# Performance work log

Measured on AMD Instinct MI355X. Metric: run time of the kernel, lower is better.

## Reference

```python
import jax, jax.numpy as jnp
import numpy as np

N, E, G = 100000, 800000, 1
DV, DE, DU, H = 64, 32, 32, 128

def _w(key, shape):
    return jax.random.normal(key, shape, dtype=jnp.float32) * 0.05

def setup_inputs() -> dict:
    key = jax.random.key(0)
    ks = jax.random.split(key, 16)
    inp = {
        "node_attr": jax.random.normal(ks[0], (N, DV), dtype=jnp.float32),
        "edges": jax.random.randint(ks[1], (2, E), 0, N, dtype=jnp.int64 if jax.config.jax_enable_x64 else jnp.int32),
        "edge_attr": jax.random.normal(ks[2], (E, DE), dtype=jnp.float32),
        "u": jax.random.normal(ks[3], (G, DU), dtype=jnp.float32),
        "node_idx": jnp.zeros((N,), dtype=jnp.int32),
        "edge_idx": jnp.zeros((E,), dtype=jnp.int32),
        # edge MLP: concat(src, dst, edge_attr, u) -> H -> H
        "W1e": _w(ks[4], (2 * DV + DE + DU, H)), "b1e": jnp.zeros((H,), jnp.float32),
        "W2e": _w(ks[5], (H, H)), "b2e": jnp.zeros((H,), jnp.float32),
        # node MLP: concat(node_attr, aggregated_edges, u) -> H -> H
        "W1n": _w(ks[6], (DV + H + DU, H)), "b1n": jnp.zeros((H,), jnp.float32),
        "W2n": _w(ks[7], (H, H)), "b2n": jnp.zeros((H,), jnp.float32),
        # global MLP: concat(node_mean, edge_mean, u) -> H -> H
        "W1g": _w(ks[8], (H + H + DU, H)), "b1g": jnp.zeros((H,), jnp.float32),
        "W2g": _w(ks[9], (H, H)), "b2g": jnp.zeros((H,), jnp.float32),
    }
    return inp

def _mlp(x, W1, b1, W2, b2):
    return jax.nn.relu(x @ W1 + b1) @ W2 + b2

def _seg_mean(x, seg, num):
    s = jax.ops.segment_sum(x, seg, num_segments=num)
    c = jax.ops.segment_sum(jnp.ones((x.shape[0], 1), x.dtype), seg, num_segments=num)
    return s / jnp.maximum(c, 1.0)

def reference(node_attr, edges, edge_attr, u, node_idx, edge_idx,
              W1e, b1e, W2e, b2e, W1n, b1n, W2n, b2n, W1g, b1g, W2g, b2g):
    row, col = edges[0], edges[1]
    # edge model: gather endpoint features, concat with edge/global attrs
    e_in = jnp.concatenate([node_attr[row], node_attr[col], edge_attr, u[edge_idx]], axis=-1)
    e = _mlp(e_in, W1e, b1e, W2e, b2e)                        # [E, H]
    # node model: scatter-add incoming edge messages onto receivers (col)
    agg = jax.ops.segment_sum(e, col, num_segments=node_attr.shape[0])  # [N, H]
    v_in = jnp.concatenate([node_attr, agg, u[node_idx]], axis=-1)
    v = _mlp(v_in, W1n, b1n, W2n, b2n)                        # [N, H]
    # global model: per-graph mean pooling of nodes and edges
    nv = _seg_mean(v, node_idx, u.shape[0])                   # [G, H]
    ne = _seg_mean(e, edge_idx, u.shape[0])                   # [G, H]
    g_in = jnp.concatenate([nv, ne, u], axis=-1)
    g = _mlp(g_in, W1g, b1g, W2g, b2g)                        # [G, H]
    return v, e, g
```

## Files before the change

kernel.cpp:

```cpp
#include <hip/hip_runtime.h>

#define N_NODES 100000
#define N_EDGES 800000
#define DV 64
#define DE 32
#define DU 32
#define H 128

#define ETILE 128
#define NTILES_E (N_EDGES / ETILE)

typedef short bf16x8 __attribute__((ext_vector_type(8)));
typedef unsigned short u16;
typedef u16 u16x8 __attribute__((ext_vector_type(8)));
typedef float f32x4 __attribute__((ext_vector_type(4)));

#define OFF_ESUM 0
#define OFF_VSUM 8192
#define OFF_BIAS 16384
#define OFF_PART 17408
#define OFF_WBUF 19456
#define OFF_DEG  175104
#define OFF_OFFS 575104
#define OFF_BUCK 975104

#define W1ET_OFF 0
#define W2ET_OFF 20480
#define W1NT_OFF 36864
#define W2NT_OFF 61440
#define WBUF_ELEMS 77824

#define NPART 391

__device__ inline u16 f2bf(float x) {
  union { float f; unsigned u; } c; c.f = x;
  unsigned r = c.u + 0x7FFFu + ((c.u >> 16) & 1u);
  return (u16)(r >> 16);
}

__global__ void prep_weights(const float* __restrict__ W1e, const float* __restrict__ W2e,
                             const float* __restrict__ W1n, const float* __restrict__ W2n,
                             u16* __restrict__ wbuf) {
  int i = blockIdx.x * blockDim.x + threadIdx.x;
  if (i < 20480) {
    int j = i / 160, k = i - j * 160;
    wbuf[W1ET_OFF + i] = f2bf(W1e[k * H + j]);
  } else if (i < 36864) {
    int t = i - 20480; int j = t >> 7, k = t & 127;
    wbuf[i] = f2bf(W2e[k * H + j]);
  } else if (i < 61440) {
    int t = i - 36864; int j = t / 192, k = t - j * 192;
    wbuf[i] = f2bf(W1n[k * H + j]);
  } else if (i < WBUF_ELEMS) {
    int t = i - 61440; int j = t >> 7, k = t & 127;
    wbuf[i] = f2bf(W2n[k * H + j]);
  }
}

__global__ void prep_bias(const float* __restrict__ uattr,
                          const float* __restrict__ W1e, const float* __restrict__ b1e,
                          const float* __restrict__ W1n, const float* __restrict__ b1n,
                          float* __restrict__ bias) {
  int t = threadIdx.x;
  float be = b1e[t];
  float bn = b1n[t];
  for (int k = 0; k < DU; ++k) {
    float uk = uattr[k];
    be += uk * W1e[(2 * DV + DE + k) * H + t];
    bn += uk * W1n[(DV + H + k) * H + t];
  }
  bias[t] = be;
  bias[128 + t] = bn;
}

__global__ void degree_kernel(const int* __restrict__ edges, int* __restrict__ deg) {
  int i = blockIdx.x * 256 + threadIdx.x;
  if (i < N_EDGES) atomicAdd(&deg[edges[N_EDGES + i]], 1);
}

__global__ void scan_part(const int* __restrict__ deg, int* __restrict__ part) {
  int i = blockIdx.x * 256 + threadIdx.x;
  int v = (i < N_NODES) ? deg[i] : 0;
#pragma unroll
  for (int m = 1; m < 64; m <<= 1) v += __shfl_xor(v, m);
  __shared__ int s[4];
  if ((threadIdx.x & 63) == 0) s[threadIdx.x >> 6] = v;
  __syncthreads();
  if (threadIdx.x == 0) part[blockIdx.x] = s[0] + s[1] + s[2] + s[3];
}

__global__ void scan_top(int* __restrict__ part) {
  __shared__ int s[512];
  int t = threadIdx.x;
  s[t] = (t < NPART) ? part[t] : 0;
  __syncthreads();
  for (int d = 1; d < 512; d <<= 1) {
    int v = (t >= d) ? s[t - d] : 0;
    __syncthreads();
    s[t] += v;
    __syncthreads();
  }
  if (t < NPART) part[t] = (t == 0) ? 0 : s[t - 1];
}

__global__ void scan_down(const int* __restrict__ part, int* __restrict__ deg_cursor,
                          int* __restrict__ offsets) {
  __shared__ int s[256];
  int b = blockIdx.x, t = threadIdx.x;
  int i = b * 256 + t;
  int v = (i < N_NODES) ? deg_cursor[i] : 0;
  s[t] = v;
  __syncthreads();
  for (int d = 1; d < 256; d <<= 1) {
    int u = (t >= d) ? s[t - d] : 0;
    __syncthreads();
    s[t] += u;
    __syncthreads();
  }
  int excl = s[t] - v + part[b];
  if (i < N_NODES) { offsets[i] = excl; deg_cursor[i] = excl; }
}

__global__ void fill_kernel(const int* __restrict__ edges, int* __restrict__ cursor,
                            int* __restrict__ bucket) {
  int i = blockIdx.x * 256 + threadIdx.x;
  if (i < N_EDGES) {
    int d = edges[N_EDGES + i];
    int pos = atomicAdd(&cursor[d], 1);
    bucket[pos] = i;
  }
}

__global__ __launch_bounds__(512, 2) void edge_kernel(
    const float* __restrict__ node_attr, const int* __restrict__ edges,
    const float* __restrict__ edge_attr,
    const u16* __restrict__ wbuf, const float* __restrict__ bias_f,
    const float* __restrict__ b2,
    float* __restrict__ e_out, float* __restrict__ esum_p)
{
  __shared__ __align__(16) char smem[75776];
  u16 (*X)[164]    = (u16(*)[164])smem;
  u16 (*Hs)[132]   = (u16(*)[132])(smem + 41984);
  float (*OT)[132] = (float(*)[132])smem;
  __shared__ int sSrc[128], sDst[128];

  const int tid = threadIdx.x;
  const int wave = tid >> 6, lane = tid & 63;
  const int l15 = lane & 15, lg = lane >> 4;
  const int wc = (wave & 3) * 32;
  const int rh = (wave >> 2) * 64;
  const long e0 = (long)blockIdx.x * ETILE;

  if (tid < 128)       sSrc[tid]       = edges[e0 + tid];
  else if (tid < 256)  sDst[tid - 128] = edges[(long)N_EDGES + e0 + (tid - 128)];

  bf16x8 w1[5][2];
  {
    const u16* w1t = wbuf + W1ET_OFF;
#pragma unroll
    for (int cf = 0; cf < 2; ++cf) {
      const u16* p1 = w1t + (wc + cf * 16 + l15) * 160 + lg * 8;
#pragma unroll
      for (int ks = 0; ks < 5; ++ks) w1[ks][cf] = *(const bf16x8*)(p1 + ks * 32);
    }
  }
  float bias1[2] = { bias_f[wc + l15], bias_f[wc + 16 + l15] };

  __syncthreads();

  {
    float4 g0[5], g1[5];
    int r_[5], c_[5];
#pragma unroll
    for (int it = 0; it < 5; ++it) {
      int ch = tid + it * 512;
      int r = ch / 20, gseg = ch - r * 20;
      int col = gseg * 8;
      r_[it] = r; c_[it] = col;
      const float* src;
      if (col < 64)        src = node_attr + (long)sSrc[r] * DV + col;
      else if (col < 128)  src = node_attr + (long)sDst[r] * DV + (col - 64);
      else                 src = edge_attr + (e0 + r) * DE + (col - 128);
      g0[it] = *(const float4*)src;
      g1[it] = *(const float4*)(src + 4);
    }
#pragma unroll
    for (int it = 0; it < 5; ++it) {
      u16x8 p;
      p[0] = f2bf(g0[it].x); p[1] = f2bf(g0[it].y); p[2] = f2bf(g0[it].z); p[3] = f2bf(g0[it].w);
      p[4] = f2bf(g1[it].x); p[5] = f2bf(g1[it].y); p[6] = f2bf(g1[it].z); p[7] = f2bf(g1[it].w);
      *(u16x8*)&X[r_[it]][c_[it]] = p;
    }
  }

  __syncthreads();

  f32x4 acc[4][2];
#pragma unroll
  for (int rf = 0; rf < 4; ++rf)
#pragma unroll
    for (int cf = 0; cf < 2; ++cf)
#pragma unroll
      for (int j = 0; j < 4; ++j) acc[rf][cf][j] = 0.f;

#pragma unroll
  for (int ks = 0; ks < 5; ++ks) {
#pragma unroll
    for (int rf = 0; rf < 4; ++rf) {
      bf16x8 a = *(const bf16x8*)&X[rh + rf * 16 + l15][ks * 32 + lg * 8];
      acc[rf][0] = __builtin_amdgcn_mfma_f32_16x16x32_bf16(a, w1[ks][0], acc[rf][0], 0, 0, 0);
      acc[rf][1] = __builtin_amdgcn_mfma_f32_16x16x32_bf16(a, w1[ks][1], acc[rf][1], 0, 0, 0);
    }
  }

  bf16x8 w2[4][2];
  {
    const u16* w2t = wbuf + W2ET_OFF;
#pragma unroll
    for (int cf = 0; cf < 2; ++cf) {
      const u16* p2 = w2t + (wc + cf * 16 + l15) * 128 + lg * 8;
#pragma unroll
      for (int ks = 0; ks < 4; ++ks) w2[ks][cf] = *(const bf16x8*)(p2 + ks * 32);
    }
  }
  float bias2[2] = { b2[wc + l15], b2[wc + 16 + l15] };

#pragma unroll
  for (int rf = 0; rf < 4; ++rf)
#pragma unroll
    for (int cf = 0; cf < 2; ++cf)
#pragma unroll
      for (int j = 0; j < 4; ++j) {
        float hv = acc[rf][cf][j] + bias1[cf];
        hv = hv > 0.f ? hv : 0.f;
        Hs[rh + rf * 16 + lg * 4 + j][wc + cf * 16 + l15] = f2bf(hv);
      }

  __syncthreads();

#pragma unroll
  for (int rf = 0; rf < 4; ++rf)
#pragma unroll
    for (int cf = 0; cf < 2; ++cf)
#pragma unroll
      for (int j = 0; j < 4; ++j) acc[rf][cf][j] = 0.f;

#pragma unroll
  for (int ks = 0; ks < 4; ++ks) {
#pragma unroll
    for (int rf = 0; rf < 4; ++rf) {
      bf16x8 a = *(const bf16x8*)&Hs[rh + rf * 16 + l15][ks * 32 + lg * 8];
      acc[rf][0] = __builtin_amdgcn_mfma_f32_16x16x32_bf16(a, w2[ks][0], acc[rf][0], 0, 0, 0);
      acc[rf][1] = __builtin_amdgcn_mfma_f32_16x16x32_bf16(a, w2[ks][1], acc[rf][1], 0, 0, 0);
    }
  }

  __syncthreads();

  float es0 = 0.f, es1 = 0.f;
#pragma unroll
  for (int rf = 0; rf < 4; ++rf) {
#pragma unroll
    for (int cf = 0; cf < 2; ++cf) {
#pragma unroll
      for (int j = 0; j < 4; ++j) {
        float v = acc[rf][cf][j] + bias2[cf];
        OT[rh + rf * 16 + lg * 4 + j][wc + cf * 16 + l15] = v;
        if (cf == 0) es0 += v; else es1 += v;
      }
    }
  }

  __syncthreads();

#pragma unroll
  for (int i = 0; i < 8; ++i) {
    int ch = tid + i * 512;
    int r = ch >> 5, c4 = ch & 31;
    float4 f = *(const float4*)&OT[r][c4 * 4];
    *(float4*)(e_out + (e0 + r) * H + c4 * 4) = f;
  }

#pragma unroll
  for (int m = 16; m < 64; m <<= 1) { es0 += __shfl_xor(es0, m); es1 += __shfl_xor(es1, m); }
  if (lane < 16) {
    atomicAdd(&esum_p[(wc + lane) * 16], es0);
    atomicAdd(&esum_p[(wc + 16 + lane) * 16], es1);
  }
}

__global__ __launch_bounds__(512, 2) void node_kernel(
    const float* __restrict__ node_attr, const u16* __restrict__ wbuf,
    const float* __restrict__ bias_f, const float* __restrict__ b2,
    const float* __restrict__ e_out, const int* __restrict__ offsets,
    const int* __restrict__ cursor, const int* __restrict__ bucket,
    float* __restrict__ v_out, float* __restrict__ vsum_p)
{
  __shared__ __align__(16) u16 X[64][196];
  __shared__ __align__(16) u16 Hs[64][132];

  const int tid = threadIdx.x;
  const int wave = tid >> 6, lane = tid & 63;
  const int l15 = lane & 15, lg = lane >> 4;
  const int wc = (wave & 3) * 32;
  const int rh = (wave >> 2) * 32;
  const long n0 = (long)blockIdx.x * 64;

  {
    int gr = tid >> 3, gs = tid & 7;
    long gn = n0 + gr; if (gn >= N_NODES) gn = N_NODES - 1;
    float a[16];
#pragma unroll
    for (int k = 0; k < 16; ++k) a[k] = 0.f;
    int s = offsets[gn], e = cursor[gn];
    int i = s;
    for (; i + 2 <= e; i += 2) {
      const float* p0 = e_out + (long)bucket[i] * H + gs * 16;
      const float* p1 = e_out + (long)bucket[i + 1] * H + gs * 16;
      float4 f0[4], f1[4];
#pragma unroll
      for (int k = 0; k < 4; ++k) f0[k] = *(const float4*)(p0 + k * 4);
#pragma unroll
      for (int k = 0; k < 4; ++k) f1[k] = *(const float4*)(p1 + k * 4);
#pragma unroll
      for (int k = 0; k < 4; ++k) {
        a[k * 4 + 0] += f0[k].x + f1[k].x;
        a[k * 4 + 1] += f0[k].y + f1[k].y;
        a[k * 4 + 2] += f0[k].z + f1[k].z;
        a[k * 4 + 3] += f0[k].w + f1[k].w;
      }
    }
    if (i < e) {
      const float* p0 = e_out + (long)bucket[i] * H + gs * 16;
#pragma unroll
      for (int k = 0; k < 4; ++k) {
        float4 f = *(const float4*)(p0 + k * 4);
        a[k * 4 + 0] += f.x; a[k * 4 + 1] += f.y;
        a[k * 4 + 2] += f.z; a[k * 4 + 3] += f.w;
      }
    }
#pragma unroll
    for (int k = 0; k < 2; ++k) {
      u16x8 pk;
#pragma unroll
      for (int j = 0; j < 8; ++j) pk[j] = f2bf(a[k * 8 + j]);
      *(u16x8*)&X[gr][64 + gs * 16 + k * 8] = pk;
    }
  }

  {
    int r = tid >> 3, col = (tid & 7) * 8;
    long n = n0 + r; if (n >= N_NODES) n = N_NODES - 1;
    const float* src = node_attr + n * DV + col;
    float4 f0 = *(const float4*)src;
    float4 f1 = *(const float4*)(src + 4);
    u16x8 p;
    p[0] = f2bf(f0.x); p[1] = f2bf(f0.y); p[2] = f2bf(f0.z); p[3] = f2bf(f0.w);
    p[4] = f2bf(f1.x); p[5] = f2bf(f1.y); p[6] = f2bf(f1.z); p[7] = f2bf(f1.w);
    *(u16x8*)&X[r][col] = p;
  }

  bf16x8 w1[6][2], w2[4][2];
  {
    const u16* w1t = wbuf + W1NT_OFF;
    const u16* w2t = wbuf + W2NT_OFF;
#pragma unroll
    for (int cf = 0; cf < 2; ++cf) {
      const u16* p1 = w1t + (wc + cf * 16 + l15) * 192 + lg * 8;
#pragma unroll
      for (int ks = 0; ks < 6; ++ks) w1[ks][cf] = *(const bf16x8*)(p1 + ks * 32);
      const u16* p2 = w2t + (wc + cf * 16 + l15) * 128 + lg * 8;
#pragma unroll
      for (int ks = 0; ks < 4; ++ks) w2[ks][cf] = *(const bf16x8*)(p2 + ks * 32);
    }
  }

  __syncthreads();

  f32x4 acc[2][2];
#pragma unroll
  for (int rf = 0; rf < 2; ++rf)
#pragma unroll
    for (int cf = 0; cf < 2; ++cf)
#pragma unroll
      for (int j = 0; j < 4; ++j) acc[rf][cf][j] = 0.f;

#pragma unroll
  for (int ks = 0; ks < 6; ++ks) {
#pragma unroll
    for (int rf = 0; rf < 2; ++rf) {
      bf16x8 a = *(const bf16x8*)&X[rh + rf * 16 + l15][ks * 32 + lg * 8];
      acc[rf][0] = __builtin_amdgcn_mfma_f32_16x16x32_bf16(a, w1[ks][0], acc[rf][0], 0, 0, 0);
      acc[rf][1] = __builtin_amdgcn_mfma_f32_16x16x32_bf16(a, w1[ks][1], acc[rf][1], 0, 0, 0);
    }
  }

  float bias1[2] = { bias_f[128 + wc + l15], bias_f[128 + wc + 16 + l15] };
#pragma unroll
  for (int rf = 0; rf < 2; ++rf)
#pragma unroll
    for (int cf = 0; cf < 2; ++cf)
#pragma unroll
      for (int j = 0; j < 4; ++j) {
        float hv = acc[rf][cf][j] + bias1[cf];
        hv = hv > 0.f ? hv : 0.f;
        Hs[rh + rf * 16 + lg * 4 + j][wc + cf * 16 + l15] = f2bf(hv);
      }

  __syncthreads();

#pragma unroll
  for (int rf = 0; rf < 2; ++rf)
#pragma unroll
    for (int cf = 0; cf < 2; ++cf)
#pragma unroll
      for (int j = 0; j < 4; ++j) acc[rf][cf][j] = 0.f;

#pragma unroll
  for (int ks = 0; ks < 4; ++ks) {
#pragma unroll
    for (int rf = 0; rf < 2; ++rf) {
      bf16x8 a = *(const bf16x8*)&Hs[rh + rf * 16 + l15][ks * 32 + lg * 8];
      acc[rf][0] = __builtin_amdgcn_mfma_f32_16x16x32_bf16(a, w2[ks][0], acc[rf][0], 0, 0, 0);
      acc[rf][1] = __builtin_amdgcn_mfma_f32_16x16x32_bf16(a, w2[ks][1], acc[rf][1], 0, 0, 0);
    }
  }

  float bias2[2] = { b2[wc + l15], b2[wc + 16 + l15] };
  float vs0 = 0.f, vs1 = 0.f;
#pragma unroll
  for (int rf = 0; rf < 2; ++rf) {
#pragma unroll
    for (int cf = 0; cf < 2; ++cf) {
      int colg = wc + cf * 16 + l15;
#pragma unroll
      for (int j = 0; j < 4; ++j) {
        int r = rh + rf * 16 + lg * 4 + j;
        long n = n0 + r;
        if (n < N_NODES) {
          float v = acc[rf][cf][j] + bias2[cf];
          v_out[n * H + colg] = v;
          if (cf == 0) vs0 += v; else vs1 += v;
        }
      }
    }
  }
#pragma unroll
  for (int m = 16; m < 64; m <<= 1) { vs0 += __shfl_xor(vs0, m); vs1 += __shfl_xor(vs1, m); }
  if (lane < 16) {
    atomicAdd(&vsum_p[(wc + lane) * 16], vs0);
    atomicAdd(&vsum_p[(wc + 16 + lane) * 16], vs1);
  }
}

__global__ void global_kernel(const float* __restrict__ uattr,
    const float* __restrict__ W1g, const float* __restrict__ b1g,
    const float* __restrict__ W2g, const float* __restrict__ b2g,
    const float* __restrict__ esum_p, const float* __restrict__ vsum_p,
    float* __restrict__ g_out)
{
  __shared__ float gin[288];
  __shared__ float hbuf[128];
  int t = threadIdx.x;
  gin[t]       = vsum_p[t * 16] * (1.f / (float)N_NODES);
  gin[128 + t] = esum_p[t * 16] * (1.f / (float)N_EDGES);
  if (t < 32) gin[256 + t] = uattr[t];
  __syncthreads();
  float a = b1g[t];
  for (int k = 0; k < 288; ++k) a += gin[k] * W1g[k * H + t];
  hbuf[t] = fmaxf(a, 0.f);
  __syncthreads();
  float b = b2g[t];
  for (int k = 0; k < 128; ++k) b += hbuf[k] * W2g[k * H + t];
  g_out[t] = b;
}

extern "C" void kernel_launch(void* const* d_in, const int* in_sizes, int n_in,
                              void* d_out, int out_size, void* d_ws, size_t ws_size,
                              hipStream_t stream) {
  const float* node_attr = (const float*)d_in[0];
  const int*   edges     = (const int*)d_in[1];
  const float* edge_attr = (const float*)d_in[2];
  const float* uattr     = (const float*)d_in[3];
  const float* W1e = (const float*)d_in[6];  const float* b1e = (const float*)d_in[7];
  const float* W2e = (const float*)d_in[8];  const float* b2e = (const float*)d_in[9];
  const float* W1n = (const float*)d_in[10]; const float* b1n = (const float*)d_in[11];
  const float* W2n = (const float*)d_in[12]; const float* b2n = (const float*)d_in[13];
  const float* W1g = (const float*)d_in[14]; const float* b1g = (const float*)d_in[15];
  const float* W2g = (const float*)d_in[16]; const float* b2g = (const float*)d_in[17];

  float* out   = (float*)d_out;
  float* v_out = out;
  float* e_out = out + (long)N_NODES * H;
  float* g_out = out + (long)N_NODES * H + (long)N_EDGES * H;

  char* ws = (char*)d_ws;
  float* esum_p = (float*)(ws + OFF_ESUM);
  float* vsum_p = (float*)(ws + OFF_VSUM);
  float* bias_f = (float*)(ws + OFF_BIAS);
  int*   part   = (int*)(ws + OFF_PART);
  u16*   wbuf   = (u16*)(ws + OFF_WBUF);
  int*   deg    = (int*)(ws + OFF_DEG);
  int*   offs   = (int*)(ws + OFF_OFFS);
  int*   buck   = (int*)(ws + OFF_BUCK);

  hipMemsetAsync(ws, 0, 16384, stream);
  hipMemsetAsync(deg, 0, N_NODES * sizeof(int), stream);

  prep_weights<<<WBUF_ELEMS / 256, 256, 0, stream>>>(W1e, W2e, W1n, W2n, wbuf);
  prep_bias<<<1, 128, 0, stream>>>(uattr, W1e, b1e, W1n, b1n, bias_f);
  degree_kernel<<<(N_EDGES + 255) / 256, 256, 0, stream>>>(edges, deg);
  scan_part<<<NPART, 256, 0, stream>>>(deg, part);
  scan_top<<<1, 512, 0, stream>>>(part);
  scan_down<<<NPART, 256, 0, stream>>>(part, deg, offs);
  fill_kernel<<<(N_EDGES + 255) / 256, 256, 0, stream>>>(edges, deg, buck);

  edge_kernel<<<NTILES_E, 512, 0, stream>>>(node_attr, edges, edge_attr, wbuf,
                                            bias_f, b2e, e_out, esum_p);
  node_kernel<<<(N_NODES + 63) / 64, 512, 0, stream>>>(node_attr, wbuf,
                                                       bias_f, b2n,
                                                       e_out, offs, deg, buck,
                                                       v_out, vsum_p);
  global_kernel<<<1, 128, 0, stream>>>(uattr, W1g, b1g, W2g, b2g, esum_p, vsum_p, g_out);
}
```

Before: 626.5 us.

## Write bf16 copy of edge messages for cheaper gather in node aggregation

The edge kernel now also writes a bf16 copy of the edge outputs to workspace, when the workspace is large enough, and the node kernel gathers from this half-size copy instead of the fp32 e_out. Streaming loads and stores are marked nontemporal to reduce cache pollution. This trades an extra 200MB write for halving the random-gather read traffic, and adds bf16 rounding error to the aggregated messages. It depends on ws_size being large enough; otherwise it falls back to the old path.

```diff
diff --git a/kernel.cpp b/kernel.cpp
--- a/kernel.cpp
+++ b/kernel.cpp
@@ -13,6 +13,7 @@
 typedef short bf16x8 __attribute__((ext_vector_type(8)));
 typedef unsigned short u16;
 typedef u16 u16x8 __attribute__((ext_vector_type(8)));
+typedef u16 u16x4 __attribute__((ext_vector_type(4)));
 typedef float f32x4 __attribute__((ext_vector_type(4)));
 
 #define OFF_ESUM 0
@@ -23,6 +24,8 @@
 #define OFF_DEG  175104
 #define OFF_OFFS 575104
 #define OFF_BUCK 975104
+#define OFF_ECOPY 4175168
+#define WS_NEED_ECOPY (4175168UL + 204800000UL)
 
 #define W1ET_OFF 0
 #define W2ET_OFF 20480
@@ -36,6 +39,9 @@
   union { float f; unsigned u; } c; c.f = x;
   unsigned r = c.u + 0x7FFFu + ((c.u >> 16) & 1u);
   return (u16)(r >> 16);
+}
+__device__ inline float bf2f(u16 h) {
+  union { unsigned u; float f; } c; c.u = (unsigned)h << 16; return c.f;
 }
 
 __global__ void prep_weights(const float* __restrict__ W1e, const float* __restrict__ W2e,
@@ -136,7 +142,8 @@
     const float* __restrict__ edge_attr,
     const u16* __restrict__ wbuf, const float* __restrict__ bias_f,
     const float* __restrict__ b2,
-    float* __restrict__ e_out, float* __restrict__ esum_p)
+    float* __restrict__ e_out, u16* __restrict__ ecopy,
+    float* __restrict__ esum_p)
 {
   __shared__ __align__(16) char smem[75776];
   u16 (*X)[164]    = (u16(*)[164])smem;
@@ -169,7 +176,7 @@
   __syncthreads();
 
   {
-    float4 g0[5], g1[5];
+    f32x4 g0[5], g1[5];
     int r_[5], c_[5];
 #pragma unroll
     for (int it = 0; it < 5; ++it) {
@@ -177,18 +184,22 @@
       int r = ch / 20, gseg = ch - r * 20;
       int col = gseg * 8;
       r_[it] = r; c_[it] = col;
-      const float* src;
-      if (col < 64)        src = node_attr + (long)sSrc[r] * DV + col;
-      else if (col < 128)  src = node_attr + (long)sDst[r] * DV + (col - 64);
-      else                 src = edge_attr + (e0 + r) * DE + (col - 128);
-      g0[it] = *(const float4*)src;
-      g1[it] = *(const float4*)(src + 4);
+      if (col < 128) {
+        const float* src = (col < 64) ? node_attr + (long)sSrc[r] * DV + col
+                                      : node_attr + (long)sDst[r] * DV + (col - 64);
+        g0[it] = *(const f32x4*)src;
+        g1[it] = *(const f32x4*)(src + 4);
+      } else {
+        const float* src = edge_attr + (e0 + r) * DE + (col - 128);
+        g0[it] = __builtin_nontemporal_load((const f32x4*)src);
+        g1[it] = __builtin_nontemporal_load((const f32x4*)(src + 4));
+      }
     }
 #pragma unroll
     for (int it = 0; it < 5; ++it) {
       u16x8 p;
-      p[0] = f2bf(g0[it].x); p[1] = f2bf(g0[it].y); p[2] = f2bf(g0[it].z); p[3] = f2bf(g0[it].w);
-      p[4] = f2bf(g1[it].x); p[5] = f2bf(g1[it].y); p[6] = f2bf(g1[it].z); p[7] = f2bf(g1[it].w);
+      p[0] = f2bf(g0[it][0]); p[1] = f2bf(g0[it][1]); p[2] = f2bf(g0[it][2]); p[3] = f2bf(g0[it][3]);
+      p[4] = f2bf(g1[it][0]); p[5] = f2bf(g1[it][1]); p[6] = f2bf(g1[it][2]); p[7] = f2bf(g1[it][3]);
       *(u16x8*)&X[r_[it]][c_[it]] = p;
     }
   }
@@ -277,8 +288,13 @@
   for (int i = 0; i < 8; ++i) {
     int ch = tid + i * 512;
     int r = ch >> 5, c4 = ch & 31;
-    float4 f = *(const float4*)&OT[r][c4 * 4];
-    *(float4*)(e_out + (e0 + r) * H + c4 * 4) = f;
+    f32x4 f = *(const f32x4*)&OT[r][c4 * 4];
+    __builtin_nontemporal_store(f, (f32x4*)(e_out + (e0 + r) * H + c4 * 4));
+    if (ecopy) {
+      u16x4 pk;
+      pk[0] = f2bf(f[0]); pk[1] = f2bf(f[1]); pk[2] = f2bf(f[2]); pk[3] = f2bf(f[3]);
+      __builtin_nontemporal_store(pk, (u16x4*)(ecopy + (e0 + r) * H + c4 * 4));
+    }
   }
 
 #pragma unroll
@@ -292,8 +308,9 @@
 __global__ __launch_bounds__(512, 2) void node_kernel(
     const float* __restrict__ node_attr, const u16* __restrict__ wbuf,
     const float* __restrict__ bias_f, const float* __restrict__ b2,
-    const float* __restrict__ e_out, const int* __restrict__ offsets,
-    const int* __restrict__ cursor, const int* __restrict__ bucket,
+    const float* __restrict__ e_out, const u16* __restrict__ ecopy,
+    const int* __restrict__ offsets, const int* __restrict__ cursor,
+    const int* __restrict__ bucket,
     float* __restrict__ v_out, float* __restrict__ vsum_p)
 {
   __shared__ __align__(16) u16 X[64][196];
@@ -313,30 +330,54 @@
 #pragma unroll
     for (int k = 0; k < 16; ++k) a[k] = 0.f;
     int s = offsets[gn], e = cursor[gn];
-    int i = s;
-    for (; i + 2 <= e; i += 2) {
-      const float* p0 = e_out + (long)bucket[i] * H + gs * 16;
-      const float* p1 = e_out + (long)bucket[i + 1] * H + gs * 16;
-      float4 f0[4], f1[4];
-#pragma unroll
-      for (int k = 0; k < 4; ++k) f0[k] = *(const float4*)(p0 + k * 4);
-#pragma unroll
-      for (int k = 0; k < 4; ++k) f1[k] = *(const float4*)(p1 + k * 4);
-#pragma unroll
-      for (int k = 0; k < 4; ++k) {
-        a[k * 4 + 0] += f0[k].x + f1[k].x;
-        a[k * 4 + 1] += f0[k].y + f1[k].y;
-        a[k * 4 + 2] += f0[k].z + f1[k].z;
-        a[k * 4 + 3] += f0[k].w + f1[k].w;
-      }
-    }
-    if (i < e) {
-      const float* p0 = e_out + (long)bucket[i] * H + gs * 16;
-#pragma unroll
-      for (int k = 0; k < 4; ++k) {
-        float4 f = *(const float4*)(p0 + k * 4);
-        a[k * 4 + 0] += f.x; a[k * 4 + 1] += f.y;
-        a[k * 4 + 2] += f.z; a[k * 4 + 3] += f.w;
+    if (ecopy) {
+      int i = s;
+      for (; i + 2 <= e; i += 2) {
+        const u16* p0 = ecopy + (long)bucket[i] * H + gs * 16;
+        const u16* p1 = ecopy + (long)bucket[i + 1] * H + gs * 16;
+        u16x8 A0 = __builtin_nontemporal_load((const u16x8*)p0);
+        u16x8 A1 = __builtin_nontemporal_load((const u16x8*)(p0 + 8));
+        u16x8 B0 = __builtin_nontemporal_load((const u16x8*)p1);
+        u16x8 B1 = __builtin_nontemporal_load((const u16x8*)(p1 + 8));
+#pragma unroll
+        for (int k = 0; k < 8; ++k) {
+          a[k]     += bf2f(A0[k]) + bf2f(B0[k]);
+          a[8 + k] += bf2f(A1[k]) + bf2f(B1[k]);
+        }
+      }
+      if (i < e) {
+        const u16* p0 = ecopy + (long)bucket[i] * H + gs * 16;
+        u16x8 A0 = __builtin_nontemporal_load((const u16x8*)p0);
+        u16x8 A1 = __builtin_nontemporal_load((const u16x8*)(p0 + 8));
+#pragma unroll
+        for (int k = 0; k < 8; ++k) { a[k] += bf2f(A0[k]); a[8 + k] += bf2f(A1[k]); }
+      }
+    } else {
+      int i = s;
+      for (; i + 2 <= e; i += 2) {
+        const float* p0 = e_out + (long)bucket[i] * H + gs * 16;
+        const float* p1 = e_out + (long)bucket[i + 1] * H + gs * 16;
+        float4 f0[4], f1[4];
+#pragma unroll
+        for (int k = 0; k < 4; ++k) f0[k] = *(const float4*)(p0 + k * 4);
+#pragma unroll
+        for (int k = 0; k < 4; ++k) f1[k] = *(const float4*)(p1 + k * 4);
+#pragma unroll
+        for (int k = 0; k < 4; ++k) {
+          a[k * 4 + 0] += f0[k].x + f1[k].x;
+          a[k * 4 + 1] += f0[k].y + f1[k].y;
+          a[k * 4 + 2] += f0[k].z + f1[k].z;
+          a[k * 4 + 3] += f0[k].w + f1[k].w;
+        }
+      }
+      if (i < e) {
+        const float* p0 = e_out + (long)bucket[i] * H + gs * 16;
+#pragma unroll
+        for (int k = 0; k < 4; ++k) {
+          float4 f = *(const float4*)(p0 + k * 4);
+          a[k * 4 + 0] += f.x; a[k * 4 + 1] += f.y;
+          a[k * 4 + 2] += f.z; a[k * 4 + 3] += f.w;
+        }
       }
     }
 #pragma unroll
@@ -439,7 +480,7 @@
         long n = n0 + r;
         if (n < N_NODES) {
           float v = acc[rf][cf][j] + bias2[cf];
-          v_out[n * H + colg] = v;
+          __builtin_nontemporal_store(v, &v_out[n * H + colg]);
           if (cf == 0) vs0 += v; else vs1 += v;
         }
       }
@@ -503,6 +544,7 @@
   int*   deg    = (int*)(ws + OFF_DEG);
   int*   offs   = (int*)(ws + OFF_OFFS);
   int*   buck   = (int*)(ws + OFF_BUCK);
+  u16*   ecopy  = (ws_size >= WS_NEED_ECOPY) ? (u16*)(ws + OFF_ECOPY) : (u16*)0;
 
   hipMemsetAsync(ws, 0, 16384, stream);
   hipMemsetAsync(deg, 0, N_NODES * sizeof(int), stream);
@@ -516,10 +558,10 @@
   fill_kernel<<<(N_EDGES + 255) / 256, 256, 0, stream>>>(edges, deg, buck);
 
   edge_kernel<<<NTILES_E, 512, 0, stream>>>(node_attr, edges, edge_attr, wbuf,
-                                            bias_f, b2e, e_out, esum_p);
+                                            bias_f, b2e, e_out, ecopy, esum_p);
   node_kernel<<<(N_NODES + 63) / 64, 512, 0, stream>>>(node_attr, wbuf,
                                                        bias_f, b2n,
-                                                       e_out, offs, deg, buck,
+                                                       e_out, ecopy, offs, deg, buck,
                                                        v_out, vsum_p);
   global_kernel<<<1, 128, 0, stream>>>(uattr, W1g, b1g, W2g, b2g, esum_p, vsum_p, g_out);
 }
```

Measured after the change: 629.9 us. Within noise of the previous version (+0.5%).

## Gather edge MLP inputs directly into MFMA registers with smaller 64-edge tiles

Applied to the files above, without the earlier changes.

The edge kernel now uses 64-edge tiles with 256 threads and drops the shared-memory staging of the concatenated input. Each lane loads its own node/edge feature fragments from global memory straight into MFMA operand registers. The output staging tile is also removed, so results are written to global memory directly from the accumulators. This cuts shared-memory use and barriers so more blocks fit per CU, but every wave now re-gathers the same input rows and the output stores become scalar, strided 4-byte writes instead of coalesced float4 rows.

```diff
diff --git a/kernel.cpp b/kernel.cpp
--- a/kernel.cpp
+++ b/kernel.cpp
@@ -7,8 +7,7 @@
 #define DU 32
 #define H 128
 
-#define ETILE 128
-#define NTILES_E (N_EDGES / ETILE)
+#define NTILES_E (N_EDGES / 64)
 
 typedef short bf16x8 __attribute__((ext_vector_type(8)));
 typedef unsigned short u16;
@@ -131,69 +130,40 @@
   }
 }
 
-__global__ __launch_bounds__(512, 2) void edge_kernel(
+__global__ __launch_bounds__(256, 3) void edge_kernel(
     const float* __restrict__ node_attr, const int* __restrict__ edges,
     const float* __restrict__ edge_attr,
     const u16* __restrict__ wbuf, const float* __restrict__ bias_f,
     const float* __restrict__ b2,
     float* __restrict__ e_out, float* __restrict__ esum_p)
 {
-  __shared__ __align__(16) char smem[75776];
-  u16 (*X)[164]    = (u16(*)[164])smem;
-  u16 (*Hs)[132]   = (u16(*)[132])(smem + 41984);
-  float (*OT)[132] = (float(*)[132])smem;
-  __shared__ int sSrc[128], sDst[128];
+  __shared__ __align__(16) u16 Hs[64][132];
 
   const int tid = threadIdx.x;
   const int wave = tid >> 6, lane = tid & 63;
   const int l15 = lane & 15, lg = lane >> 4;
-  const int wc = (wave & 3) * 32;
-  const int rh = (wave >> 2) * 64;
-  const long e0 = (long)blockIdx.x * ETILE;
-
-  if (tid < 128)       sSrc[tid]       = edges[e0 + tid];
-  else if (tid < 256)  sDst[tid - 128] = edges[(long)N_EDGES + e0 + (tid - 128)];
+  const int kc = lg * 8;
+  const int wc = wave * 32;
+  const long e0 = (long)blockIdx.x * 64;
 
   bf16x8 w1[5][2];
   {
     const u16* w1t = wbuf + W1ET_OFF;
 #pragma unroll
     for (int cf = 0; cf < 2; ++cf) {
-      const u16* p1 = w1t + (wc + cf * 16 + l15) * 160 + lg * 8;
+      const u16* p1 = w1t + (wc + cf * 16 + l15) * 160 + kc;
 #pragma unroll
       for (int ks = 0; ks < 5; ++ks) w1[ks][cf] = *(const bf16x8*)(p1 + ks * 32);
     }
   }
   float bias1[2] = { bias_f[wc + l15], bias_f[wc + 16 + l15] };
 
-  __syncthreads();
-
-  {
-    float4 g0[5], g1[5];
-    int r_[5], c_[5];
-#pragma unroll
-    for (int it = 0; it < 5; ++it) {
-      int ch = tid + it * 512;
-      int r = ch / 20, gseg = ch - r * 20;
-      int col = gseg * 8;
-      r_[it] = r; c_[it] = col;
-      const float* src;
-      if (col < 64)        src = node_attr + (long)sSrc[r] * DV + col;
-      else if (col < 128)  src = node_attr + (long)sDst[r] * DV + (col - 64);
-      else                 src = edge_attr + (e0 + r) * DE + (col - 128);
-      g0[it] = *(const float4*)src;
-      g1[it] = *(const float4*)(src + 4);
-    }
-#pragma unroll
-    for (int it = 0; it < 5; ++it) {
-      u16x8 p;
-      p[0] = f2bf(g0[it].x); p[1] = f2bf(g0[it].y); p[2] = f2bf(g0[it].z); p[3] = f2bf(g0[it].w);
-      p[4] = f2bf(g1[it].x); p[5] = f2bf(g1[it].y); p[6] = f2bf(g1[it].z); p[7] = f2bf(g1[it].w);
-      *(u16x8*)&X[r_[it]][c_[it]] = p;
-    }
-  }
-
-  __syncthreads();
+  int sid[4], did[4];
+#pragma unroll
+  for (int rf = 0; rf < 4; ++rf) {
+    sid[rf] = edges[e0 + rf * 16 + l15];
+    did[rf] = edges[(long)N_EDGES + e0 + rf * 16 + l15];
+  }
 
   f32x4 acc[4][2];
 #pragma unroll
@@ -205,80 +175,86 @@
 
 #pragma unroll
   for (int ks = 0; ks < 5; ++ks) {
+    f32x4 ga[4], gb[4];
 #pragma unroll
     for (int rf = 0; rf < 4; ++rf) {
-      bf16x8 a = *(const bf16x8*)&X[rh + rf * 16 + l15][ks * 32 + lg * 8];
-      acc[rf][0] = __builtin_amdgcn_mfma_f32_16x16x32_bf16(a, w1[ks][0], acc[rf][0], 0, 0, 0);
-      acc[rf][1] = __builtin_amdgcn_mfma_f32_16x16x32_bf16(a, w1[ks][1], acc[rf][1], 0, 0, 0);
-    }
-  }
+      const float* p;
+      if (ks == 0)      p = node_attr + (long)sid[rf] * DV + kc;
+      else if (ks == 1) p = node_attr + (long)sid[rf] * DV + 32 + kc;
+      else if (ks == 2) p = node_attr + (long)did[rf] * DV + kc;
+      else if (ks == 3) p = node_attr + (long)did[rf] * DV + 32 + kc;
+      else              p = edge_attr + (e0 + rf * 16 + l15) * DE + kc;
+      ga[rf] = *(const f32x4*)p;
+      gb[rf] = *(const f32x4*)(p + 4);
+    }
+#pragma unroll
+    for (int rf = 0; rf < 4; ++rf) {
+      u16x8 a;
+      a[0] = f2bf(ga[rf][0]); a[1] = f2bf(ga[rf][1]);
+      a[2] = f2bf(ga[rf][2]); a[3] = f2bf(ga[rf][3]);
+      a[4] = f2bf(gb[rf][0]); a[5] = f2bf(gb[rf][1]);
+      a[6] = f2bf(gb[rf][2]); a[7] = f2bf(gb[rf][3]);
+      acc[rf][0] = __builtin_amdgcn_mfma_f32_16x16x32_bf16((bf16x8)a, w1[ks][0], acc[rf][0], 0, 0, 0);
+      acc[rf][1] = __builtin_amdgcn_mfma_f32_16x16x32_bf16((bf16x8)a, w1[ks][1], acc[rf][1], 0, 0, 0);
+    }
+  }
+
+#pragma unroll
+  for (int rf = 0; rf < 4; ++rf)
+#pragma unroll
+    for (int cf = 0; cf < 2; ++cf)
+#pragma unroll
+      for (int j = 0; j < 4; ++j) {
+        float hv = acc[rf][cf][j] + bias1[cf];
+        hv = hv > 0.f ? hv : 0.f;
+        Hs[rf * 16 + lg * 4 + j][wc + cf * 16 + l15] = f2bf(hv);
+      }
 
   bf16x8 w2[4][2];
   {
     const u16* w2t = wbuf + W2ET_OFF;
 #pragma unroll
     for (int cf = 0; cf < 2; ++cf) {
-      const u16* p2 = w2t + (wc + cf * 16 + l15) * 128 + lg * 8;
+      const u16* p2 = w2t + (wc + cf * 16 + l15) * 128 + kc;
 #pragma unroll
       for (int ks = 0; ks < 4; ++ks) w2[ks][cf] = *(const bf16x8*)(p2 + ks * 32);
     }
   }
   float bias2[2] = { b2[wc + l15], b2[wc + 16 + l15] };
 
+  __syncthreads();
+
 #pragma unroll
   for (int rf = 0; rf < 4; ++rf)
 #pragma unroll
     for (int cf = 0; cf < 2; ++cf)
 #pragma unroll
-      for (int j = 0; j < 4; ++j) {
-        float hv = acc[rf][cf][j] + bias1[cf];
-        hv = hv > 0.f ? hv : 0.f;
-        Hs[rh + rf * 16 + lg * 4 + j][wc + cf * 16 + l15] = f2bf(hv);
-      }
-
-  __syncthreads();
-
-#pragma unroll
-  for (int rf = 0; rf < 4; ++rf)
-#pragma unroll
-    for (int cf = 0; cf < 2; ++cf)
-#pragma unroll
       for (int j = 0; j < 4; ++j) acc[rf][cf][j] = 0.f;
 
 #pragma unroll
   for (int ks = 0; ks < 4; ++ks) {
 #pragma unroll
     for (int rf = 0; rf < 4; ++rf) {
-      bf16x8 a = *(const bf16x8*)&Hs[rh + rf * 16 + l15][ks * 32 + lg * 8];
+      bf16x8 a = *(const bf16x8*)&Hs[rf * 16 + l15][ks * 32 + kc];
       acc[rf][0] = __builtin_amdgcn_mfma_f32_16x16x32_bf16(a, w2[ks][0], acc[rf][0], 0, 0, 0);
       acc[rf][1] = __builtin_amdgcn_mfma_f32_16x16x32_bf16(a, w2[ks][1], acc[rf][1], 0, 0, 0);
     }
   }
 
-  __syncthreads();
-
   float es0 = 0.f, es1 = 0.f;
 #pragma unroll
   for (int rf = 0; rf < 4; ++rf) {
 #pragma unroll
     for (int cf = 0; cf < 2; ++cf) {
+      int colg = wc + cf * 16 + l15;
 #pragma unroll
       for (int j = 0; j < 4; ++j) {
         float v = acc[rf][cf][j] + bias2[cf];
-        OT[rh + rf * 16 + lg * 4 + j][wc + cf * 16 + l15] = v;
+        long r = rf * 16 + lg * 4 + j;
+        e_out[(e0 + r) * H + colg] = v;
         if (cf == 0) es0 += v; else es1 += v;
       }
     }
-  }
-
-  __syncthreads();
-
-#pragma unroll
-  for (int i = 0; i < 8; ++i) {
-    int ch = tid + i * 512;
-    int r = ch >> 5, c4 = ch & 31;
-    float4 f = *(const float4*)&OT[r][c4 * 4];
-    *(float4*)(e_out + (e0 + r) * H + c4 * 4) = f;
   }
 
 #pragma unroll
@@ -515,7 +491,7 @@
   scan_down<<<NPART, 256, 0, stream>>>(part, deg, offs);
   fill_kernel<<<(N_EDGES + 255) / 256, 256, 0, stream>>>(edges, deg, buck);
 
-  edge_kernel<<<NTILES_E, 512, 0, stream>>>(node_attr, edges, edge_attr, wbuf,
+  edge_kernel<<<NTILES_E, 256, 0, stream>>>(node_attr, edges, edge_attr, wbuf,
                                             bias_f, b2e, e_out, esum_p);
   node_kernel<<<(N_NODES + 63) / 64, 512, 0, stream>>>(node_attr, wbuf,
                                                        bias_f, b2n,
```

Measured after the change: 666.9 us. 6.4% more time.

## Alias shared-memory buffers and split output staging to raise occupancy

Applied to the files above, without the earlier changes.

Both the edge and node kernels now overlay their X, Hs and output-staging tiles on one shared slab, with extra barriers between phases. In the edge kernel the output transpose is done in two 64-row halves so the staging area fits in the smaller slab. Launch bounds go from 2 to 6 blocks per CU so more workgroups can be resident to hide gather latency. The cost is extra __syncthreads, serialized output staging, and a tighter register budget that may cause spills.

```diff
diff --git a/kernel.cpp b/kernel.cpp
--- a/kernel.cpp
+++ b/kernel.cpp
@@ -131,17 +131,17 @@
   }
 }
 
-__global__ __launch_bounds__(512, 2) void edge_kernel(
+__global__ __launch_bounds__(512, 6) void edge_kernel(
     const float* __restrict__ node_attr, const int* __restrict__ edges,
     const float* __restrict__ edge_attr,
     const u16* __restrict__ wbuf, const float* __restrict__ bias_f,
     const float* __restrict__ b2,
     float* __restrict__ e_out, float* __restrict__ esum_p)
 {
-  __shared__ __align__(16) char smem[75776];
-  u16 (*X)[164]    = (u16(*)[164])smem;
-  u16 (*Hs)[132]   = (u16(*)[132])(smem + 41984);
-  float (*OT)[132] = (float(*)[132])smem;
+  __shared__ __align__(16) char slab[41984];
+  u16 (*X)[164]    = (u16(*)[164])slab;
+  u16 (*Hs)[132]   = (u16(*)[132])slab;
+  float (*OT)[132] = (float(*)[132])slab;
   __shared__ int sSrc[128], sDst[128];
 
   const int tid = threadIdx.x;
@@ -169,26 +169,26 @@
   __syncthreads();
 
   {
-    float4 g0[5], g1[5];
+    f32x4 g0[5], g1[5];
     int r_[5], c_[5];
 #pragma unroll
     for (int it = 0; it < 5; ++it) {
       int ch = tid + it * 512;
-      int r = ch / 20, gseg = ch - r * 20;
-      int col = gseg * 8;
+      int r = ch / 20, seg = ch - r * 20;
+      int col = seg * 8;
       r_[it] = r; c_[it] = col;
       const float* src;
       if (col < 64)        src = node_attr + (long)sSrc[r] * DV + col;
       else if (col < 128)  src = node_attr + (long)sDst[r] * DV + (col - 64);
       else                 src = edge_attr + (e0 + r) * DE + (col - 128);
-      g0[it] = *(const float4*)src;
-      g1[it] = *(const float4*)(src + 4);
+      g0[it] = *(const f32x4*)src;
+      g1[it] = *(const f32x4*)(src + 4);
     }
 #pragma unroll
     for (int it = 0; it < 5; ++it) {
       u16x8 p;
-      p[0] = f2bf(g0[it].x); p[1] = f2bf(g0[it].y); p[2] = f2bf(g0[it].z); p[3] = f2bf(g0[it].w);
-      p[4] = f2bf(g1[it].x); p[5] = f2bf(g1[it].y); p[6] = f2bf(g1[it].z); p[7] = f2bf(g1[it].w);
+      p[0] = f2bf(g0[it][0]); p[1] = f2bf(g0[it][1]); p[2] = f2bf(g0[it][2]); p[3] = f2bf(g0[it][3]);
+      p[4] = f2bf(g1[it][0]); p[5] = f2bf(g1[it][1]); p[6] = f2bf(g1[it][2]); p[7] = f2bf(g1[it][3]);
       *(u16x8*)&X[r_[it]][c_[it]] = p;
     }
   }
@@ -225,6 +225,8 @@
   }
   float bias2[2] = { b2[wc + l15], b2[wc + 16 + l15] };
 
+  __syncthreads();
+
 #pragma unroll
   for (int rf = 0; rf < 4; ++rf)
 #pragma unroll
@@ -258,28 +260,53 @@
   __syncthreads();
 
   float es0 = 0.f, es1 = 0.f;
-#pragma unroll
-  for (int rf = 0; rf < 4; ++rf) {
-#pragma unroll
-    for (int cf = 0; cf < 2; ++cf) {
-#pragma unroll
-      for (int j = 0; j < 4; ++j) {
-        float v = acc[rf][cf][j] + bias2[cf];
-        OT[rh + rf * 16 + lg * 4 + j][wc + cf * 16 + l15] = v;
-        if (cf == 0) es0 += v; else es1 += v;
-      }
-    }
-  }
-
-  __syncthreads();
-
-#pragma unroll
-  for (int i = 0; i < 8; ++i) {
+
+  if (rh == 0) {
+#pragma unroll
+    for (int rf = 0; rf < 4; ++rf) {
+#pragma unroll
+      for (int cf = 0; cf < 2; ++cf) {
+#pragma unroll
+        for (int j = 0; j < 4; ++j) {
+          float v = acc[rf][cf][j] + bias2[cf];
+          OT[rf * 16 + lg * 4 + j][wc + cf * 16 + l15] = v;
+          if (cf == 0) es0 += v; else es1 += v;
+        }
+      }
+    }
+  }
+  __syncthreads();
+#pragma unroll
+  for (int i = 0; i < 4; ++i) {
     int ch = tid + i * 512;
     int r = ch >> 5, c4 = ch & 31;
     float4 f = *(const float4*)&OT[r][c4 * 4];
     *(float4*)(e_out + (e0 + r) * H + c4 * 4) = f;
   }
+  __syncthreads();
+
+  if (rh == 64) {
+#pragma unroll
+    for (int rf = 0; rf < 4; ++rf) {
+#pragma unroll
+      for (int cf = 0; cf < 2; ++cf) {
+#pragma unroll
+        for (int j = 0; j < 4; ++j) {
+          float v = acc[rf][cf][j] + bias2[cf];
+          OT[rf * 16 + lg * 4 + j][wc + cf * 16 + l15] = v;
+          if (cf == 0) es0 += v; else es1 += v;
+        }
+      }
+    }
+  }
+  __syncthreads();
+#pragma unroll
+  for (int i = 0; i < 4; ++i) {
+    int ch = tid + i * 512;
+    int r = ch >> 5, c4 = ch & 31;
+    float4 f = *(const float4*)&OT[r][c4 * 4];
+    *(float4*)(e_out + (e0 + 64 + r) * H + c4 * 4) = f;
+  }
 
 #pragma unroll
   for (int m = 16; m < 64; m <<= 1) { es0 += __shfl_xor(es0, m); es1 += __shfl_xor(es1, m); }
@@ -289,15 +316,16 @@
   }
 }
 
-__global__ __launch_bounds__(512, 2) void node_kernel(
+__global__ __launch_bounds__(512, 6) void node_kernel(
     const float* __restrict__ node_attr, const u16* __restrict__ wbuf,
     const float* __restrict__ bias_f, const float* __restrict__ b2,
     const float* __restrict__ e_out, const int* __restrict__ offsets,
     const int* __restrict__ cursor, const int* __restrict__ bucket,
     float* __restrict__ v_out, float* __restrict__ vsum_p)
 {
-  __shared__ __align__(16) u16 X[64][196];
-  __shared__ __align__(16) u16 Hs[64][132];
+  __shared__ __align__(16) char slab[25088];
+  u16 (*X)[196]  = (u16(*)[196])slab;
+  u16 (*Hs)[132] = (u16(*)[132])slab;
 
   const int tid = threadIdx.x;
   const int wave = tid >> 6, lane = tid & 63;
@@ -394,6 +422,8 @@
       acc[rf][1] = __builtin_amdgcn_mfma_f32_16x16x32_bf16(a, w1[ks][1], acc[rf][1], 0, 0, 0);
     }
   }
+
+  __syncthreads();
 
   float bias1[2] = { bias_f[128 + wc + l15], bias_f[128 + wc + 16 + l15] };
 #pragma unroll
```

After: 690.8 us. 1.1x slower.
